# Kernel tuning notes

Hardware: AMD Instinct MI355X
Metric: run time of the kernel (lower is better)

The kernel has to match this reference:

```python
import jax, jax.numpy as jnp
import numpy as np

B, S, D = 16, 1, 2048
NH, NKV = 32, 8
HD = D // NH          # 64
GRP = NH // NKV       # 4
MAX_SEQ = 4096
START = MAX_SEQ - S   # 4095
HIDDEN = 5632         # 256*ceil((2*4*D/3)/256)
EPS = 1e-6


def _rope(x, cos, sin):
    # x: [b, s, h, d]; cos/sin: [s, d//2]; llama complex rotation on pairs
    b, s, h, d = x.shape
    xr = x.reshape(b, s, h, d // 2, 2)
    x0, x1 = xr[..., 0], xr[..., 1]
    c = cos[None, :, None, :]
    sn = sin[None, :, None, :]
    o0 = x0 * c - x1 * sn
    o1 = x0 * sn + x1 * c
    return jnp.stack([o0, o1], axis=-1).reshape(b, s, h, d)


def _rmsnorm(x, w, eps=EPS):
    return w * (x * jax.lax.rsqrt(jnp.mean(x * x, axis=-1, keepdims=True) + eps))


def setup_inputs() -> dict:
    key = jax.random.key(0)
    ks = jax.random.split(key, 12)
    sc = 0.02
    pos = jnp.arange(START, START + S, dtype=jnp.float32)
    inv = 1.0 / (10000.0 ** (jnp.arange(0, HD, 2, dtype=jnp.float32) / HD))
    ang = pos[:, None] * inv[None, :]  # [S, HD//2]
    return {
        "x": jax.random.normal(ks[0], (B, S, D), jnp.float32),
        "freqs_cos": jnp.cos(ang),
        "freqs_sin": jnp.sin(ang),
        "cache_k": jax.random.normal(ks[1], (B, MAX_SEQ, NKV, HD), jnp.float32),
        "cache_v": jax.random.normal(ks[2], (B, MAX_SEQ, NKV, HD), jnp.float32),
        "wq_w": jax.random.normal(ks[3], (D, D), jnp.float32) * sc,
        "wk_w": jax.random.normal(ks[4], (NKV * HD, D), jnp.float32) * sc,
        "wv_w": jax.random.normal(ks[5], (NKV * HD, D), jnp.float32) * sc,
        "wo_w": jax.random.normal(ks[6], (D, D), jnp.float32) * sc,
        "w1_w": jax.random.normal(ks[7], (HIDDEN, D), jnp.float32) * sc,
        "w2_w": jax.random.normal(ks[8], (D, HIDDEN), jnp.float32) * sc,
        "w3_w": jax.random.normal(ks[9], (D, D), jnp.float32) * sc,
        "attn_norm_w": jnp.ones((D,), jnp.float32),
        "ffn_norm_w": jnp.ones((D,), jnp.float32),
        "start_pos": START,
    }


def reference(x, freqs_cos, freqs_sin, cache_k, cache_v, wq_w, wk_w, wv_w, wo_w,
              w1_w, w2_w, w3_w, attn_norm_w, ffn_norm_w, start_pos):
    b, s, dim = x.shape
    # --- attention ---
    xn = _rmsnorm(x, attn_norm_w)
    xq = (xn @ wq_w.T).reshape(b, s, NH, HD)
    xk = (xn @ wk_w.T).reshape(b, s, NKV, HD)
    xv = (xn @ wv_w.T).reshape(b, s, NKV, HD)
    # source applies rotary embedding to q, k AND v
    xq = _rope(xq, freqs_cos, freqs_sin)
    xk = _rope(xk, freqs_cos, freqs_sin)
    xv = _rope(xv, freqs_cos, freqs_sin)
    # KV-cache write at start_pos, read prefix
    cache_k = jax.lax.dynamic_update_slice(cache_k, xk, (0, start_pos, 0, 0))
    cache_v = jax.lax.dynamic_update_slice(cache_v, xv, (0, start_pos, 0, 0))
    T = start_pos + s
    keys = cache_k[:, :T]   # [b, T, NKV, HD]
    vals = cache_v[:, :T]
    # GQA: group q heads per kv head (equivalent to repeat_kv + matmul)
    q = xq.reshape(b, s, NKV, GRP, HD)
    scores = jnp.einsum('bsKgd,btKd->bKgst', q, keys) / jnp.sqrt(jnp.float32(HD))
    probs = jax.nn.softmax(scores.astype(jnp.float32), axis=-1).astype(xq.dtype)
    attn = jnp.einsum('bKgst,btKd->bsKgd', probs, vals).reshape(b, s, dim)
    h = x + attn @ wo_w.T
    hn = _rmsnorm(h, ffn_norm_w)
    ff = jax.nn.silu(hn @ w1_w.T) @ w2_w.T + hn @ w3_w.T
    return h + ff
```

## Files before the change

### kernel.cpp

```cpp
#include <hip/hip_runtime.h>
#include <math.h>

#define NB      16
#define DIM     2048
#define NKVh    8
#define HDIM    64
#define GRP     4
#define MAXSEQ  4096
#define TPOS    4095
#define FFH     5632
#define NSPLIT  8
#define CHUNK   512

#define XN_OFF   0
#define Q_OFF    32768
#define ATTN_OFF 65536
#define H_OFF    98304
#define HN_OFF   131072
#define H1_OFF   163840
#define H3_OFF   253952
#define PML_OFF  286720
#define PO_OFF   294912

__global__ __launch_bounds__(256) void rmsnorm_k(const float* __restrict__ x,
    const float* __restrict__ w, float* __restrict__ o) {
  int b = blockIdx.x;
  const float* xr = x + b * DIM;
  float ss = 0.f;
#pragma unroll
  for (int i = 0; i < DIM / 256; ++i) {
    float v = xr[threadIdx.x + i * 256];
    ss += v * v;
  }
#pragma unroll
  for (int m = 32; m >= 1; m >>= 1) ss += __shfl_xor(ss, m, 64);
  __shared__ float sred[4];
  if ((threadIdx.x & 63) == 0) sred[threadIdx.x >> 6] = ss;
  __syncthreads();
  float r = rsqrtf((sred[0] + sred[1] + sred[2] + sred[3]) * (1.f / DIM) + 1e-6f);
#pragma unroll
  for (int i = 0; i < DIM / 256; ++i) {
    int idx = threadIdx.x + i * 256;
    o[b * DIM + idx] = w[idx] * xr[idx] * r;
  }
}

template <int K4>
__device__ inline void gemv_core(const float* __restrict__ W,
                                 const float* __restrict__ X,
                                 int row0, float acc[4][4]) {
  const int lane = threadIdx.x & 63;
  const int wv   = threadIdx.x >> 6;
  const int lk   = lane & 15;
  const int b4   = lane >> 4;
  const float4* __restrict__ Wv = (const float4*)W;
  const float4* __restrict__ Xv = (const float4*)X;
#pragma unroll
  for (int r = 0; r < 4; ++r)
#pragma unroll
    for (int j = 0; j < 4; ++j) acc[r][j] = 0.f;

  const int half = K4 / 2;
  int k4 = wv * half + lk;
#pragma unroll 2
  for (int i = 0; i < half / 16; ++i, k4 += 16) {
    float4 xb[4];
#pragma unroll
    for (int j = 0; j < 4; ++j) xb[j] = Xv[(b4 + 4 * j) * K4 + k4];
#pragma unroll
    for (int r = 0; r < 4; ++r) {
      float4 wr = Wv[(row0 + r) * K4 + k4];
#pragma unroll
      for (int j = 0; j < 4; ++j)
        acc[r][j] += wr.x * xb[j].x + wr.y * xb[j].y + wr.z * xb[j].z + wr.w * xb[j].w;
    }
  }
#pragma unroll
  for (int m = 1; m < 16; m <<= 1)
#pragma unroll
    for (int r = 0; r < 4; ++r)
#pragma unroll
      for (int j = 0; j < 4; ++j) acc[r][j] += __shfl_xor(acc[r][j], m, 64);
  __shared__ float sred[4][4][4];
  if (wv == 1 && lk == 0) {
#pragma unroll
    for (int r = 0; r < 4; ++r)
#pragma unroll
      for (int j = 0; j < 4; ++j) sred[b4][r][j] = acc[r][j];
  }
  __syncthreads();
  if (wv == 0) {
#pragma unroll
    for (int r = 0; r < 4; ++r)
#pragma unroll
      for (int j = 0; j < 4; ++j) acc[r][j] += sred[b4][r][j];
  }
}

__global__ __launch_bounds__(128) void qkv_k(const float* __restrict__ xn,
    const float* __restrict__ wq, const float* __restrict__ wk,
    const float* __restrict__ wv, const float* __restrict__ fc,
    const float* __restrict__ fs, float* __restrict__ qo,
    float* __restrict__ ck, float* __restrict__ cv) {
  int row0 = blockIdx.x * 4;
  const float* W;
  int lr, kind;
  if (row0 < DIM)            { W = wq; lr = row0;             kind = 0; }
  else if (row0 < DIM + 512) { W = wk; lr = row0 - DIM;       kind = 1; }
  else                       { W = wv; lr = row0 - DIM - 512; kind = 2; }
  float acc[4][4];
  gemv_core<512>(W, xn, lr, acc);
  if ((threadIdx.x >> 6) != 0 || (threadIdx.x & 15) != 0) return;
  int b4 = (threadIdx.x >> 4) & 3;
  int dl = lr & 63;
  int j0 = dl >> 1;
  float c0 = fc[j0], s0 = fs[j0], c1 = fc[j0 + 1], s1 = fs[j0 + 1];
  const float QS = 0.125f * 1.44269504088896f;
#pragma unroll
  for (int j = 0; j < 4; ++j) {
    int b = b4 + 4 * j;
    float a0 = acc[0][j], a1 = acc[1][j], a2 = acc[2][j], a3 = acc[3][j];
    float o0 = a0 * c0 - a1 * s0, o1 = a0 * s0 + a1 * c0;
    float o2 = a2 * c1 - a3 * s1, o3 = a2 * s1 + a3 * c1;
    if (kind == 0) {
      float* qp = qo + b * DIM + lr;
      qp[0] = o0 * QS; qp[1] = o1 * QS; qp[2] = o2 * QS; qp[3] = o3 * QS;
    } else {
      int kvh = lr >> 6;
      float* cp = (kind == 1 ? ck : cv) +
                  (((size_t)b * MAXSEQ + TPOS) * NKVh + kvh) * HDIM + dl;
      cp[0] = o0; cp[1] = o1; cp[2] = o2; cp[3] = o3;
    }
  }
}

__global__ __launch_bounds__(256) void attn_part_k(const float* __restrict__ q,
    const float* __restrict__ ck, const float* __restrict__ cv,
    float* __restrict__ pml, float* __restrict__ po) {
  int blk = blockIdx.x;
  int sp = blk & (NSPLIT - 1);
  int bk = blk / NSPLIT;
  int kv = bk & 7, b = bk >> 3;
  int w = threadIdx.x >> 6, lane = threadIdx.x & 63;
  int tg = lane >> 4, lk = lane & 15;

  float4 q4[GRP];
#pragma unroll
  for (int g = 0; g < GRP; ++g)
    q4[g] = *(const float4*)&q[b * DIM + (kv * GRP + g) * HDIM + lk * 4];

  float m[GRP], l[GRP];
  float4 o[GRP];
#pragma unroll
  for (int g = 0; g < GRP; ++g) {
    m[g] = -1e30f; l[g] = 0.f;
    o[g].x = 0.f; o[g].y = 0.f; o[g].z = 0.f; o[g].w = 0.f;
  }
  const float4* Kb = (const float4*)ck + (size_t)b * (MAXSEQ * NKVh * HDIM / 4) + kv * (HDIM / 4);
  const float4* Vb = (const float4*)cv + (size_t)b * (MAXSEQ * NKVh * HDIM / 4) + kv * (HDIM / 4);
  int t0 = sp * CHUNK + w * 4 + tg;
#pragma unroll 2
  for (int it = 0; it < CHUNK / 16; ++it) {
    int t = t0 + it * 16;
    float4 kr = Kb[(size_t)t * (NKVh * HDIM / 4) + lk];
    float s[GRP];
#pragma unroll
    for (int g = 0; g < GRP; ++g)
      s[g] = kr.x * q4[g].x + kr.y * q4[g].y + kr.z * q4[g].z + kr.w * q4[g].w;
#pragma unroll
    for (int msk = 1; msk < 16; msk <<= 1)
#pragma unroll
      for (int g = 0; g < GRP; ++g) s[g] += __shfl_xor(s[g], msk, 64);
    float4 vr = Vb[(size_t)t * (NKVh * HDIM / 4) + lk];
#pragma unroll
    for (int g = 0; g < GRP; ++g) {
      float mn = fmaxf(m[g], s[g]);
      float sc = exp2f(m[g] - mn);
      float p  = exp2f(s[g] - mn);
      l[g] = l[g] * sc + p;
      o[g].x = o[g].x * sc + p * vr.x;
      o[g].y = o[g].y * sc + p * vr.y;
      o[g].z = o[g].z * sc + p * vr.z;
      o[g].w = o[g].w * sc + p * vr.w;
      m[g] = mn;
    }
  }
  __shared__ float sml[16][GRP][2];
  __shared__ float so[16][GRP][HDIM];
  int set = w * 4 + tg;
#pragma unroll
  for (int g = 0; g < GRP; ++g) {
    *(float4*)&so[set][g][lk * 4] = o[g];
    if (lk == 0) { sml[set][g][0] = m[g]; sml[set][g][1] = l[g]; }
  }
  __syncthreads();
  int g = threadIdx.x >> 6, d = threadIdx.x & 63;
  float M = -1e30f;
#pragma unroll
  for (int s2 = 0; s2 < 16; ++s2) M = fmaxf(M, sml[s2][g][0]);
  float L = 0.f, O = 0.f;
#pragma unroll
  for (int s2 = 0; s2 < 16; ++s2) {
    float e = exp2f(sml[s2][g][0] - M);
    L += e * sml[s2][g][1];
    O += e * so[s2][g][d];
  }
  int idx = (bk * GRP + g) * NSPLIT + sp;
  po[idx * HDIM + d] = O;
  if (d == 0) { pml[idx * 2] = M; pml[idx * 2 + 1] = L; }
}

__global__ __launch_bounds__(256) void attn_comb_k(const float* __restrict__ pml,
    const float* __restrict__ po, float* __restrict__ attn) {
  int t = blockIdx.x * 256 + threadIdx.x;
  int d = t & 63, bkg = t >> 6;
  float M = -1e30f;
#pragma unroll
  for (int sp = 0; sp < NSPLIT; ++sp) M = fmaxf(M, pml[(bkg * NSPLIT + sp) * 2]);
  float L = 0.f, O = 0.f;
#pragma unroll
  for (int sp = 0; sp < NSPLIT; ++sp) {
    float e = exp2f(pml[(bkg * NSPLIT + sp) * 2] - M);
    L += e * pml[(bkg * NSPLIT + sp) * 2 + 1];
    O += e * po[(bkg * NSPLIT + sp) * HDIM + d];
  }
  attn[bkg * HDIM + d] = O / L;
}

__global__ __launch_bounds__(128) void wo_k(const float* __restrict__ attn,
    const float* __restrict__ wo, const float* __restrict__ x,
    float* __restrict__ h) {
  int row0 = blockIdx.x * 4;
  float acc[4][4];
  gemv_core<512>(wo, attn, row0, acc);
  if ((threadIdx.x >> 6) != 0 || (threadIdx.x & 15) != 0) return;
  int b4 = (threadIdx.x >> 4) & 3;
#pragma unroll
  for (int j = 0; j < 4; ++j) {
    int b = b4 + 4 * j;
#pragma unroll
    for (int r = 0; r < 4; ++r)
      h[b * DIM + row0 + r] = x[b * DIM + row0 + r] + acc[r][j];
  }
}

__global__ __launch_bounds__(128) void ffn13_k(const float* __restrict__ hn,
    const float* __restrict__ w1, const float* __restrict__ w3,
    float* __restrict__ h1, float* __restrict__ h3) {
  int row0 = blockIdx.x * 4;
  bool is1 = row0 < FFH;
  const float* W = is1 ? w1 : w3;
  int lr = is1 ? row0 : row0 - FFH;
  float acc[4][4];
  gemv_core<512>(W, hn, lr, acc);
  if ((threadIdx.x >> 6) != 0 || (threadIdx.x & 15) != 0) return;
  int b4 = (threadIdx.x >> 4) & 3;
#pragma unroll
  for (int j = 0; j < 4; ++j) {
    int b = b4 + 4 * j;
#pragma unroll
    for (int r = 0; r < 4; ++r) {
      float v = acc[r][j];
      if (is1) h1[b * FFH + lr + r] = v / (1.f + expf(-v));
      else     h3[b * DIM + lr + r] = v;
    }
  }
}

__global__ __launch_bounds__(128) void ffn2_k(const float* __restrict__ h1,
    const float* __restrict__ w2, const float* __restrict__ h,
    const float* __restrict__ h3, float* __restrict__ out) {
  int row0 = blockIdx.x * 4;
  float acc[4][4];
  gemv_core<1408>(w2, h1, row0, acc);
  if ((threadIdx.x >> 6) != 0 || (threadIdx.x & 15) != 0) return;
  int b4 = (threadIdx.x >> 4) & 3;
#pragma unroll
  for (int j = 0; j < 4; ++j) {
    int b = b4 + 4 * j;
#pragma unroll
    for (int r = 0; r < 4; ++r)
      out[b * DIM + row0 + r] = h[b * DIM + row0 + r] + h3[b * DIM + row0 + r] + acc[r][j];
  }
}

extern "C" void kernel_launch(void* const* d_in, const int* in_sizes, int n_in,
                              void* d_out, int out_size, void* d_ws, size_t ws_size,
                              hipStream_t stream) {
  (void)in_sizes; (void)n_in; (void)out_size; (void)ws_size;
  const float* x   = (const float*)d_in[0];
  const float* fc  = (const float*)d_in[1];
  const float* fs  = (const float*)d_in[2];
  float*       ck  = (float*)d_in[3];
  float*       cv  = (float*)d_in[4];
  const float* wq  = (const float*)d_in[5];
  const float* wk  = (const float*)d_in[6];
  const float* wvp = (const float*)d_in[7];
  const float* wo  = (const float*)d_in[8];
  const float* w1  = (const float*)d_in[9];
  const float* w2  = (const float*)d_in[10];
  const float* w3  = (const float*)d_in[11];
  const float* anw = (const float*)d_in[12];
  const float* fnw = (const float*)d_in[13];
  float* ws  = (float*)d_ws;
  float* out = (float*)d_out;

  rmsnorm_k<<<NB, 256, 0, stream>>>(x, anw, ws + XN_OFF);
  qkv_k<<<(DIM + 512 + 512) / 4, 128, 0, stream>>>(ws + XN_OFF, wq, wk, wvp, fc, fs,
                                                   ws + Q_OFF, ck, cv);
  attn_part_k<<<NB * NKVh * NSPLIT, 256, 0, stream>>>(ws + Q_OFF, ck, cv,
                                                      ws + PML_OFF, ws + PO_OFF);
  attn_comb_k<<<(NB * DIM) / 256, 256, 0, stream>>>(ws + PML_OFF, ws + PO_OFF, ws + ATTN_OFF);
  wo_k<<<DIM / 4, 128, 0, stream>>>(ws + ATTN_OFF, wo, x, ws + H_OFF);
  rmsnorm_k<<<NB, 256, 0, stream>>>(ws + H_OFF, fnw, ws + HN_OFF);
  ffn13_k<<<(FFH + DIM) / 4, 128, 0, stream>>>(ws + HN_OFF, w1, w3, ws + H1_OFF, ws + H3_OFF);
  ffn2_k<<<DIM / 4, 128, 0, stream>>>(ws + H1_OFF, w2, ws + H_OFF, ws + H3_OFF, out);
}
```

Measured before the change: 476.4 us.

## Rework GEMV to single-wave 64-accumulator transpose reduction and widen attention lanes

Replaces the two-wave GEMV core with a single 64-thread wave per 4 rows. Each lane loads contiguous float4 weight chunks and accumulates all 16 batch rows, then uses a butterfly shuffle-transpose reduction so each lane ends with one output, with no shared memory or barrier. QKV, wo and FFN kernels now launch 64-thread blocks, and the RoPE epilogue uses a lane shuffle. Attention partials now assign 8 lanes per token with 8 dims each, giving a shorter shuffle reduction and 32 partial sets, at the cost of higher register pressure from 64 accumulators and fewer waves per block.

```diff
diff --git a/kernel.cpp b/kernel.cpp
--- a/kernel.cpp
+++ b/kernel.cpp
@@ -22,6 +22,10 @@
 #define PML_OFF  286720
 #define PO_OFF   294912
 
+__device__ __forceinline__ float dot4(float4 a, float4 b) {
+  return a.x * b.x + a.y * b.y + a.z * b.z + a.w * b.w;
+}
+
 __global__ __launch_bounds__(256) void rmsnorm_k(const float* __restrict__ x,
     const float* __restrict__ w, float* __restrict__ o) {
   int b = blockIdx.x;
@@ -46,58 +50,46 @@
 }
 
 template <int K4>
-__device__ inline void gemv_core(const float* __restrict__ W,
-                                 const float* __restrict__ X,
-                                 int row0, float acc[4][4]) {
+__device__ __forceinline__ float gemv64(const float* __restrict__ W,
+                                        const float* __restrict__ X, int row0) {
   const int lane = threadIdx.x & 63;
-  const int wv   = threadIdx.x >> 6;
-  const int lk   = lane & 15;
-  const int b4   = lane >> 4;
   const float4* __restrict__ Wv = (const float4*)W;
   const float4* __restrict__ Xv = (const float4*)X;
-#pragma unroll
-  for (int r = 0; r < 4; ++r)
-#pragma unroll
-    for (int j = 0; j < 4; ++j) acc[r][j] = 0.f;
-
-  const int half = K4 / 2;
-  int k4 = wv * half + lk;
+  float a[64];
+#pragma unroll
+  for (int j = 0; j < 64; ++j) a[j] = 0.f;
 #pragma unroll 2
-  for (int i = 0; i < half / 16; ++i, k4 += 16) {
-    float4 xb[4];
-#pragma unroll
-    for (int j = 0; j < 4; ++j) xb[j] = Xv[(b4 + 4 * j) * K4 + k4];
-#pragma unroll
-    for (int r = 0; r < 4; ++r) {
-      float4 wr = Wv[(row0 + r) * K4 + k4];
-#pragma unroll
-      for (int j = 0; j < 4; ++j)
-        acc[r][j] += wr.x * xb[j].x + wr.y * xb[j].y + wr.z * xb[j].z + wr.w * xb[j].w;
+  for (int it = 0; it < K4 / 64; ++it) {
+    int k = it * 64 + lane;
+    float4 w0 = Wv[(size_t)(row0 + 0) * K4 + k];
+    float4 w1 = Wv[(size_t)(row0 + 1) * K4 + k];
+    float4 w2 = Wv[(size_t)(row0 + 2) * K4 + k];
+    float4 w3 = Wv[(size_t)(row0 + 3) * K4 + k];
+#pragma unroll
+    for (int b = 0; b < 16; ++b) {
+      float4 xb = Xv[(size_t)b * K4 + k];
+      a[0 * 16 + b] += dot4(w0, xb);
+      a[1 * 16 + b] += dot4(w1, xb);
+      a[2 * 16 + b] += dot4(w2, xb);
+      a[3 * 16 + b] += dot4(w3, xb);
     }
   }
 #pragma unroll
-  for (int m = 1; m < 16; m <<= 1)
-#pragma unroll
-    for (int r = 0; r < 4; ++r)
-#pragma unroll
-      for (int j = 0; j < 4; ++j) acc[r][j] += __shfl_xor(acc[r][j], m, 64);
-  __shared__ float sred[4][4][4];
-  if (wv == 1 && lk == 0) {
-#pragma unroll
-    for (int r = 0; r < 4; ++r)
-#pragma unroll
-      for (int j = 0; j < 4; ++j) sred[b4][r][j] = acc[r][j];
-  }
-  __syncthreads();
-  if (wv == 0) {
-#pragma unroll
-    for (int r = 0; r < 4; ++r)
-#pragma unroll
-      for (int j = 0; j < 4; ++j) acc[r][j] += sred[b4][r][j];
-  }
-}
-
-__global__ __launch_bounds__(128) void qkv_k(const float* __restrict__ xn,
+  for (int s = 0; s < 6; ++s) {
+    const int m = 1 << s;
+    const int mybit = (lane >> s) & 1;
+#pragma unroll
+    for (int i = 0; i < (64 >> (s + 1)); ++i) {
+      float x0 = a[2 * i], x1 = a[2 * i + 1];
+      float keep = mybit ? x1 : x0;
+      float give = mybit ? x0 : x1;
+      a[i] = keep + __shfl_xor(give, m, 64);
+    }
+  }
+  return a[0];
+}
+
+__global__ __launch_bounds__(64) void qkv_k(const float* __restrict__ xn,
     const float* __restrict__ wq, const float* __restrict__ wk,
     const float* __restrict__ wv, const float* __restrict__ fc,
     const float* __restrict__ fs, float* __restrict__ qo,
@@ -108,29 +100,22 @@
   if (row0 < DIM)            { W = wq; lr = row0;             kind = 0; }
   else if (row0 < DIM + 512) { W = wk; lr = row0 - DIM;       kind = 1; }
   else                       { W = wv; lr = row0 - DIM - 512; kind = 2; }
-  float acc[4][4];
-  gemv_core<512>(W, xn, lr, acc);
-  if ((threadIdx.x >> 6) != 0 || (threadIdx.x & 15) != 0) return;
-  int b4 = (threadIdx.x >> 4) & 3;
-  int dl = lr & 63;
-  int j0 = dl >> 1;
-  float c0 = fc[j0], s0 = fs[j0], c1 = fc[j0 + 1], s1 = fs[j0 + 1];
+  float v = gemv64<512>(W, xn, lr);
+  float pv = __shfl_xor(v, 16, 64);
+  int lane = threadIdx.x & 63;
+  int r = lane >> 4, b = lane & 15;
+  int dl = (lr & 63) + r;
+  int jp = ((lr & 63) + (r & 2)) >> 1;
+  float c = fc[jp], sn = fs[jp];
+  float o = (r & 1) ? (pv * sn + v * c) : (v * c - pv * sn);
   const float QS = 0.125f * 1.44269504088896f;
-#pragma unroll
-  for (int j = 0; j < 4; ++j) {
-    int b = b4 + 4 * j;
-    float a0 = acc[0][j], a1 = acc[1][j], a2 = acc[2][j], a3 = acc[3][j];
-    float o0 = a0 * c0 - a1 * s0, o1 = a0 * s0 + a1 * c0;
-    float o2 = a2 * c1 - a3 * s1, o3 = a2 * s1 + a3 * c1;
-    if (kind == 0) {
-      float* qp = qo + b * DIM + lr;
-      qp[0] = o0 * QS; qp[1] = o1 * QS; qp[2] = o2 * QS; qp[3] = o3 * QS;
-    } else {
-      int kvh = lr >> 6;
-      float* cp = (kind == 1 ? ck : cv) +
-                  (((size_t)b * MAXSEQ + TPOS) * NKVh + kvh) * HDIM + dl;
-      cp[0] = o0; cp[1] = o1; cp[2] = o2; cp[3] = o3;
-    }
+  if (kind == 0) {
+    qo[b * DIM + lr + r] = o * QS;
+  } else {
+    int kvh = lr >> 6;
+    float* cp = (kind == 1 ? ck : cv) +
+                (((size_t)b * MAXSEQ + TPOS) * NKVh + kvh) * HDIM + dl;
+    *cp = o;
   }
 }
 
@@ -142,65 +127,77 @@
   int bk = blk / NSPLIT;
   int kv = bk & 7, b = bk >> 3;
   int w = threadIdx.x >> 6, lane = threadIdx.x & 63;
-  int tg = lane >> 4, lk = lane & 15;
-
-  float4 q4[GRP];
-#pragma unroll
-  for (int g = 0; g < GRP; ++g)
-    q4[g] = *(const float4*)&q[b * DIM + (kv * GRP + g) * HDIM + lk * 4];
+  int t8 = lane >> 3, d8 = lane & 7;
+
+  float4 q4[GRP][2];
+#pragma unroll
+  for (int g = 0; g < GRP; ++g) {
+    const float* qp = q + b * DIM + (kv * GRP + g) * HDIM + d8 * 8;
+    q4[g][0] = *(const float4*)qp;
+    q4[g][1] = *(const float4*)(qp + 4);
+  }
 
   float m[GRP], l[GRP];
-  float4 o[GRP];
+  float4 o0[GRP], o1[GRP];
 #pragma unroll
   for (int g = 0; g < GRP; ++g) {
     m[g] = -1e30f; l[g] = 0.f;
-    o[g].x = 0.f; o[g].y = 0.f; o[g].z = 0.f; o[g].w = 0.f;
-  }
-  const float4* Kb = (const float4*)ck + (size_t)b * (MAXSEQ * NKVh * HDIM / 4) + kv * (HDIM / 4);
-  const float4* Vb = (const float4*)cv + (size_t)b * (MAXSEQ * NKVh * HDIM / 4) + kv * (HDIM / 4);
-  int t0 = sp * CHUNK + w * 4 + tg;
+    o0[g] = make_float4(0.f, 0.f, 0.f, 0.f);
+    o1[g] = make_float4(0.f, 0.f, 0.f, 0.f);
+  }
+  const size_t bkoff = ((size_t)b * MAXSEQ * NKVh + kv) * HDIM + d8 * 8;
+  const float* Kp = ck + bkoff;
+  const float* Vp = cv + bkoff;
+  int tbase = sp * CHUNK + w * 128 + t8;
 #pragma unroll 2
-  for (int it = 0; it < CHUNK / 16; ++it) {
-    int t = t0 + it * 16;
-    float4 kr = Kb[(size_t)t * (NKVh * HDIM / 4) + lk];
+  for (int it = 0; it < 16; ++it) {
+    size_t toff = (size_t)(tbase + it * 8) * (NKVh * HDIM);
+    float4 ka = *(const float4*)(Kp + toff);
+    float4 kb = *(const float4*)(Kp + toff + 4);
     float s[GRP];
 #pragma unroll
     for (int g = 0; g < GRP; ++g)
-      s[g] = kr.x * q4[g].x + kr.y * q4[g].y + kr.z * q4[g].z + kr.w * q4[g].w;
-#pragma unroll
-    for (int msk = 1; msk < 16; msk <<= 1)
+      s[g] = dot4(ka, q4[g][0]) + dot4(kb, q4[g][1]);
+#pragma unroll
+    for (int msk = 1; msk < 8; msk <<= 1)
 #pragma unroll
       for (int g = 0; g < GRP; ++g) s[g] += __shfl_xor(s[g], msk, 64);
-    float4 vr = Vb[(size_t)t * (NKVh * HDIM / 4) + lk];
+    float4 va = *(const float4*)(Vp + toff);
+    float4 vb = *(const float4*)(Vp + toff + 4);
 #pragma unroll
     for (int g = 0; g < GRP; ++g) {
       float mn = fmaxf(m[g], s[g]);
       float sc = exp2f(m[g] - mn);
       float p  = exp2f(s[g] - mn);
       l[g] = l[g] * sc + p;
-      o[g].x = o[g].x * sc + p * vr.x;
-      o[g].y = o[g].y * sc + p * vr.y;
-      o[g].z = o[g].z * sc + p * vr.z;
-      o[g].w = o[g].w * sc + p * vr.w;
+      o0[g].x = o0[g].x * sc + p * va.x;
+      o0[g].y = o0[g].y * sc + p * va.y;
+      o0[g].z = o0[g].z * sc + p * va.z;
+      o0[g].w = o0[g].w * sc + p * va.w;
+      o1[g].x = o1[g].x * sc + p * vb.x;
+      o1[g].y = o1[g].y * sc + p * vb.y;
+      o1[g].z = o1[g].z * sc + p * vb.z;
+      o1[g].w = o1[g].w * sc + p * vb.w;
       m[g] = mn;
     }
   }
-  __shared__ float sml[16][GRP][2];
-  __shared__ float so[16][GRP][HDIM];
-  int set = w * 4 + tg;
+  __shared__ float sml[32][GRP][2];
+  __shared__ float so[32][GRP][HDIM];
+  int set = w * 8 + t8;
 #pragma unroll
   for (int g = 0; g < GRP; ++g) {
-    *(float4*)&so[set][g][lk * 4] = o[g];
-    if (lk == 0) { sml[set][g][0] = m[g]; sml[set][g][1] = l[g]; }
+    *(float4*)&so[set][g][d8 * 8]     = o0[g];
+    *(float4*)&so[set][g][d8 * 8 + 4] = o1[g];
+    if (d8 == 0) { sml[set][g][0] = m[g]; sml[set][g][1] = l[g]; }
   }
   __syncthreads();
   int g = threadIdx.x >> 6, d = threadIdx.x & 63;
   float M = -1e30f;
 #pragma unroll
-  for (int s2 = 0; s2 < 16; ++s2) M = fmaxf(M, sml[s2][g][0]);
+  for (int s2 = 0; s2 < 32; ++s2) M = fmaxf(M, sml[s2][g][0]);
   float L = 0.f, O = 0.f;
 #pragma unroll
-  for (int s2 = 0; s2 < 16; ++s2) {
+  for (int s2 = 0; s2 < 32; ++s2) {
     float e = exp2f(sml[s2][g][0] - M);
     L += e * sml[s2][g][1];
     O += e * so[s2][g][d];
@@ -227,61 +224,38 @@
   attn[bkg * HDIM + d] = O / L;
 }
 
-__global__ __launch_bounds__(128) void wo_k(const float* __restrict__ attn,
+__global__ __launch_bounds__(64) void wo_k(const float* __restrict__ attn,
     const float* __restrict__ wo, const float* __restrict__ x,
     float* __restrict__ h) {
   int row0 = blockIdx.x * 4;
-  float acc[4][4];
-  gemv_core<512>(wo, attn, row0, acc);
-  if ((threadIdx.x >> 6) != 0 || (threadIdx.x & 15) != 0) return;
-  int b4 = (threadIdx.x >> 4) & 3;
-#pragma unroll
-  for (int j = 0; j < 4; ++j) {
-    int b = b4 + 4 * j;
-#pragma unroll
-    for (int r = 0; r < 4; ++r)
-      h[b * DIM + row0 + r] = x[b * DIM + row0 + r] + acc[r][j];
-  }
-}
-
-__global__ __launch_bounds__(128) void ffn13_k(const float* __restrict__ hn,
+  float v = gemv64<512>(wo, attn, row0);
+  int lane = threadIdx.x & 63;
+  int r = lane >> 4, b = lane & 15;
+  h[b * DIM + row0 + r] = x[b * DIM + row0 + r] + v;
+}
+
+__global__ __launch_bounds__(64) void ffn13_k(const float* __restrict__ hn,
     const float* __restrict__ w1, const float* __restrict__ w3,
     float* __restrict__ h1, float* __restrict__ h3) {
   int row0 = blockIdx.x * 4;
   bool is1 = row0 < FFH;
   const float* W = is1 ? w1 : w3;
   int lr = is1 ? row0 : row0 - FFH;
-  float acc[4][4];
-  gemv_core<512>(W, hn, lr, acc);
-  if ((threadIdx.x >> 6) != 0 || (threadIdx.x & 15) != 0) return;
-  int b4 = (threadIdx.x >> 4) & 3;
-#pragma unroll
-  for (int j = 0; j < 4; ++j) {
-    int b = b4 + 4 * j;
-#pragma unroll
-    for (int r = 0; r < 4; ++r) {
-      float v = acc[r][j];
-      if (is1) h1[b * FFH + lr + r] = v / (1.f + expf(-v));
-      else     h3[b * DIM + lr + r] = v;
-    }
-  }
-}
-
-__global__ __launch_bounds__(128) void ffn2_k(const float* __restrict__ h1,
+  float v = gemv64<512>(W, hn, lr);
+  int lane = threadIdx.x & 63;
+  int r = lane >> 4, b = lane & 15;
+  if (is1) h1[b * FFH + lr + r] = v / (1.f + expf(-v));
+  else     h3[b * DIM + lr + r] = v;
+}
+
+__global__ __launch_bounds__(64) void ffn2_k(const float* __restrict__ h1,
     const float* __restrict__ w2, const float* __restrict__ h,
     const float* __restrict__ h3, float* __restrict__ out) {
   int row0 = blockIdx.x * 4;
-  float acc[4][4];
-  gemv_core<1408>(w2, h1, row0, acc);
-  if ((threadIdx.x >> 6) != 0 || (threadIdx.x & 15) != 0) return;
-  int b4 = (threadIdx.x >> 4) & 3;
-#pragma unroll
-  for (int j = 0; j < 4; ++j) {
-    int b = b4 + 4 * j;
-#pragma unroll
-    for (int r = 0; r < 4; ++r)
-      out[b * DIM + row0 + r] = h[b * DIM + row0 + r] + h3[b * DIM + row0 + r] + acc[r][j];
-  }
+  float v = gemv64<1408>(w2, h1, row0);
+  int lane = threadIdx.x & 63;
+  int r = lane >> 4, b = lane & 15;
+  out[b * DIM + row0 + r] = h[b * DIM + row0 + r] + h3[b * DIM + row0 + r] + v;
 }
 
 extern "C" void kernel_launch(void* const* d_in, const int* in_sizes, int n_in,
@@ -306,13 +280,13 @@
   float* out = (float*)d_out;
 
   rmsnorm_k<<<NB, 256, 0, stream>>>(x, anw, ws + XN_OFF);
-  qkv_k<<<(DIM + 512 + 512) / 4, 128, 0, stream>>>(ws + XN_OFF, wq, wk, wvp, fc, fs,
-                                                   ws + Q_OFF, ck, cv);
+  qkv_k<<<(DIM + 512 + 512) / 4, 64, 0, stream>>>(ws + XN_OFF, wq, wk, wvp, fc, fs,
+                                                  ws + Q_OFF, ck, cv);
   attn_part_k<<<NB * NKVh * NSPLIT, 256, 0, stream>>>(ws + Q_OFF, ck, cv,
                                                       ws + PML_OFF, ws + PO_OFF);
   attn_comb_k<<<(NB * DIM) / 256, 256, 0, stream>>>(ws + PML_OFF, ws + PO_OFF, ws + ATTN_OFF);
-  wo_k<<<DIM / 4, 128, 0, stream>>>(ws + ATTN_OFF, wo, x, ws + H_OFF);
+  wo_k<<<DIM / 4, 64, 0, stream>>>(ws + ATTN_OFF, wo, x, ws + H_OFF);
   rmsnorm_k<<<NB, 256, 0, stream>>>(ws + H_OFF, fnw, ws + HN_OFF);
-  ffn13_k<<<(FFH + DIM) / 4, 128, 0, stream>>>(ws + HN_OFF, w1, w3, ws + H1_OFF, ws + H3_OFF);
-  ffn2_k<<<DIM / 4, 128, 0, stream>>>(ws + H1_OFF, w2, ws + H_OFF, ws + H3_OFF, out);
-}
+  ffn13_k<<<(FFH + DIM) / 4, 64, 0, stream>>>(ws + HN_OFF, w1, w3, ws + H1_OFF, ws + H3_OFF);
+  ffn2_k<<<DIM / 4, 64, 0, stream>>>(ws + H1_OFF, w2, ws + H_OFF, ws + H3_OFF, out);
+}
```

Measured after the change: 525.2 us. +10.3%, slower.

## Stage KV cache through LDS with async loads and double-buffer GEMV loads

Applied to the files above, without the earlier changes.

Attention partials now run one 512-thread block per (batch, split), covering all 8 KV heads. Each block copies contiguous K/V rows into a 4-deep LDS ring using global_load_lds, overlapping with compute via vmcnt waits and barriers. The GEMV core is rewritten with explicit software pipelining that alternates two register sets of weight and activation loads. The aims are fully coalesced cache reads and hidden memory latency, at the cost of far fewer attention blocks (256), 64KB of LDS per block and more register pressure.

```diff
diff --git a/kernel.cpp b/kernel.cpp
--- a/kernel.cpp
+++ b/kernel.cpp
@@ -9,8 +9,9 @@
 #define MAXSEQ  4096
 #define TPOS    4095
 #define FFH     5632
-#define NSPLIT  8
-#define CHUNK   512
+#define NSPLIT  16
+#define TSPAN   256
+#define TROW    512
 
 #define XN_OFF   0
 #define Q_OFF    32768
@@ -20,7 +21,18 @@
 #define H1_OFF   163840
 #define H3_OFF   253952
 #define PML_OFF  286720
-#define PO_OFF   294912
+#define PO_OFF   303104
+
+__device__ __forceinline__ float dot4(float4 a, float4 b) {
+  return a.x * b.x + a.y * b.y + a.z * b.z + a.w * b.w;
+}
+
+#define GLOAD_LDS(srcp, ldsp)                                                  \
+  __builtin_amdgcn_global_load_lds(                                            \
+      (const __attribute__((address_space(1))) void*)(srcp),                   \
+      (__attribute__((address_space(3))) void*)(ldsp), 16, 0, 0)
+
+#define WAITBAR(N) asm volatile("s_waitcnt vmcnt(" #N ")\n\ts_barrier" ::: "memory")
 
 __global__ __launch_bounds__(256) void rmsnorm_k(const float* __restrict__ x,
     const float* __restrict__ w, float* __restrict__ o) {
@@ -46,9 +58,9 @@
 }
 
 template <int K4>
-__device__ inline void gemv_core(const float* __restrict__ W,
-                                 const float* __restrict__ X,
-                                 int row0, float acc[4][4]) {
+__device__ __forceinline__ void gemv_core(const float* __restrict__ W,
+                                          const float* __restrict__ X,
+                                          int row0, float acc[4][4]) {
   const int lane = threadIdx.x & 63;
   const int wv   = threadIdx.x >> 6;
   const int lk   = lane & 15;
@@ -59,22 +71,41 @@
   for (int r = 0; r < 4; ++r)
 #pragma unroll
     for (int j = 0; j < 4; ++j) acc[r][j] = 0.f;
-
-  const int half = K4 / 2;
-  int k4 = wv * half + lk;
-#pragma unroll 2
-  for (int i = 0; i < half / 16; ++i, k4 += 16) {
-    float4 xb[4];
-#pragma unroll
-    for (int j = 0; j < 4; ++j) xb[j] = Xv[(b4 + 4 * j) * K4 + k4];
-#pragma unroll
-    for (int r = 0; r < 4; ++r) {
-      float4 wr = Wv[(row0 + r) * K4 + k4];
-#pragma unroll
-      for (int j = 0; j < 4; ++j)
-        acc[r][j] += wr.x * xb[j].x + wr.y * xb[j].y + wr.z * xb[j].z + wr.w * xb[j].w;
-    }
-  }
+  constexpr int NI = K4 / 32;
+  const int k0 = wv * (K4 / 2) + lk;
+  float4 aw0, aw1, aw2, aw3, ax0, ax1, ax2, ax3;
+  float4 bw0, bw1, bw2, bw3, bx0, bx1, bx2, bx3;
+#define LDA(S, it) { int kk = k0 + (it) * 16;                                  \
+    S##w0 = Wv[(size_t)(row0 + 0) * K4 + kk];                                  \
+    S##w1 = Wv[(size_t)(row0 + 1) * K4 + kk];                                  \
+    S##w2 = Wv[(size_t)(row0 + 2) * K4 + kk];                                  \
+    S##w3 = Wv[(size_t)(row0 + 3) * K4 + kk];                                  \
+    S##x0 = Xv[(size_t)(b4 + 0) * K4 + kk];                                    \
+    S##x1 = Xv[(size_t)(b4 + 4) * K4 + kk];                                    \
+    S##x2 = Xv[(size_t)(b4 + 8) * K4 + kk];                                    \
+    S##x3 = Xv[(size_t)(b4 + 12) * K4 + kk]; }
+#define FMA4(S) {                                                              \
+    acc[0][0] += dot4(S##w0, S##x0); acc[0][1] += dot4(S##w0, S##x1);          \
+    acc[0][2] += dot4(S##w0, S##x2); acc[0][3] += dot4(S##w0, S##x3);          \
+    acc[1][0] += dot4(S##w1, S##x0); acc[1][1] += dot4(S##w1, S##x1);          \
+    acc[1][2] += dot4(S##w1, S##x2); acc[1][3] += dot4(S##w1, S##x3);          \
+    acc[2][0] += dot4(S##w2, S##x0); acc[2][1] += dot4(S##w2, S##x1);          \
+    acc[2][2] += dot4(S##w2, S##x2); acc[2][3] += dot4(S##w2, S##x3);          \
+    acc[3][0] += dot4(S##w3, S##x0); acc[3][1] += dot4(S##w3, S##x1);          \
+    acc[3][2] += dot4(S##w3, S##x2); acc[3][3] += dot4(S##w3, S##x3); }
+  LDA(a, 0);
+#pragma unroll 1
+  for (int it = 0; it + 2 < NI; it += 2) {
+    LDA(b, it + 1);
+    FMA4(a);
+    LDA(a, it + 2);
+    FMA4(b);
+  }
+  LDA(b, NI - 1);
+  FMA4(a);
+  FMA4(b);
+#undef LDA
+#undef FMA4
 #pragma unroll
   for (int m = 1; m < 16; m <<= 1)
 #pragma unroll
@@ -134,80 +165,106 @@
   }
 }
 
-__global__ __launch_bounds__(256) void attn_part_k(const float* __restrict__ q,
+__global__ __launch_bounds__(512) void attn_part_k(const float* __restrict__ q,
     const float* __restrict__ ck, const float* __restrict__ cv,
     float* __restrict__ pml, float* __restrict__ po) {
-  int blk = blockIdx.x;
-  int sp = blk & (NSPLIT - 1);
-  int bk = blk / NSPLIT;
-  int kv = bk & 7, b = bk >> 3;
-  int w = threadIdx.x >> 6, lane = threadIdx.x & 63;
-  int tg = lane >> 4, lk = lane & 15;
+  __shared__ float smem[16384];
+  int sp = blockIdx.x & (NSPLIT - 1);
+  int b  = blockIdx.x >> 4;
+  int tid = threadIdx.x;
+  int w = tid >> 6, lane = tid & 63;
+  int t4 = lane >> 4, dl = lane & 15;
+
+  const float* Kg = ck + ((size_t)b * MAXSEQ + sp * TSPAN) * TROW;
+  const float* Vg = cv + ((size_t)b * MAXSEQ + sp * TSPAN) * TROW;
+  const float* Sg = (w < 4) ? Kg : Vg;
+  const int    srow = w & 3;
 
   float4 q4[GRP];
 #pragma unroll
   for (int g = 0; g < GRP; ++g)
-    q4[g] = *(const float4*)&q[b * DIM + (kv * GRP + g) * HDIM + lk * 4];
+    q4[g] = *(const float4*)(q + b * DIM + (w * GRP + g) * HDIM + dl * 4);
 
   float m[GRP], l[GRP];
   float4 o[GRP];
 #pragma unroll
   for (int g = 0; g < GRP; ++g) {
     m[g] = -1e30f; l[g] = 0.f;
-    o[g].x = 0.f; o[g].y = 0.f; o[g].z = 0.f; o[g].w = 0.f;
-  }
-  const float4* Kb = (const float4*)ck + (size_t)b * (MAXSEQ * NKVh * HDIM / 4) + kv * (HDIM / 4);
-  const float4* Vb = (const float4*)cv + (size_t)b * (MAXSEQ * NKVh * HDIM / 4) + kv * (HDIM / 4);
-  int t0 = sp * CHUNK + w * 4 + tg;
-#pragma unroll 2
-  for (int it = 0; it < CHUNK / 16; ++it) {
-    int t = t0 + it * 16;
-    float4 kr = Kb[(size_t)t * (NKVh * HDIM / 4) + lk];
-    float s[GRP];
-#pragma unroll
-    for (int g = 0; g < GRP; ++g)
-      s[g] = kr.x * q4[g].x + kr.y * q4[g].y + kr.z * q4[g].z + kr.w * q4[g].w;
-#pragma unroll
-    for (int msk = 1; msk < 16; msk <<= 1)
-#pragma unroll
-      for (int g = 0; g < GRP; ++g) s[g] += __shfl_xor(s[g], msk, 64);
-    float4 vr = Vb[(size_t)t * (NKVh * HDIM / 4) + lk];
-#pragma unroll
-    for (int g = 0; g < GRP; ++g) {
-      float mn = fmaxf(m[g], s[g]);
-      float sc = exp2f(m[g] - mn);
-      float p  = exp2f(s[g] - mn);
-      l[g] = l[g] * sc + p;
-      o[g].x = o[g].x * sc + p * vr.x;
-      o[g].y = o[g].y * sc + p * vr.y;
-      o[g].z = o[g].z * sc + p * vr.z;
-      o[g].w = o[g].w * sc + p * vr.w;
-      m[g] = mn;
+    o[g] = make_float4(0.f, 0.f, 0.f, 0.f);
+  }
+
+#define STAGE(tile) {                                                          \
+    const float* src = Sg + ((size_t)(tile) * 4 + srow) * TROW + lane * 4;     \
+    float* dst = smem + (((tile) & 3) * 4096) + ((w >= 4) ? 2048 : 0) +        \
+                 srow * TROW;                                                  \
+    GLOAD_LDS(src, dst);                                                       \
+    GLOAD_LDS(src + 256, dst + 256); }
+
+#define COMPUTE(tile) {                                                        \
+    const float* bb = smem + (((tile) & 3) * 4096) + t4 * TROW + w * 64 + dl * 4; \
+    float4 ka = *(const float4*)bb;                                            \
+    float4 va = *(const float4*)(bb + 2048);                                   \
+    float s_[GRP];                                                             \
+    _Pragma("unroll") for (int g = 0; g < GRP; ++g) s_[g] = dot4(ka, q4[g]);   \
+    _Pragma("unroll") for (int msk = 1; msk < 16; msk <<= 1)                   \
+      _Pragma("unroll") for (int g = 0; g < GRP; ++g)                          \
+        s_[g] += __shfl_xor(s_[g], msk, 64);                                   \
+    _Pragma("unroll") for (int g = 0; g < GRP; ++g) {                          \
+      float mn = fmaxf(m[g], s_[g]);                                           \
+      float sc = exp2f(m[g] - mn);                                             \
+      float p  = exp2f(s_[g] - mn);                                            \
+      l[g] = l[g] * sc + p;                                                    \
+      o[g].x = o[g].x * sc + p * va.x;                                         \
+      o[g].y = o[g].y * sc + p * va.y;                                         \
+      o[g].z = o[g].z * sc + p * va.z;                                         \
+      o[g].w = o[g].w * sc + p * va.w;                                         \
+      m[g] = mn; } }
+
+  STAGE(0);
+  STAGE(1);
+#pragma unroll 1
+  for (int t = 0; t < 62; ++t) {
+    STAGE(t + 2);
+    WAITBAR(4);
+    COMPUTE(t);
+  }
+  WAITBAR(2);
+  COMPUTE(62);
+  WAITBAR(0);
+  COMPUTE(63);
+#undef STAGE
+#undef COMPUTE
+
+  __syncthreads();
+  float* so  = smem;
+  float* sml = smem + 8192;
+#pragma unroll
+  for (int g = 0; g < GRP; ++g) {
+    *(float4*)&so[(((w * 4 + t4) * GRP) + g) * 64 + dl * 4] = o[g];
+    if (dl == 0) {
+      sml[(((w * 4 + t4) * GRP) + g) * 2]     = m[g];
+      sml[(((w * 4 + t4) * GRP) + g) * 2 + 1] = l[g];
     }
   }
-  __shared__ float sml[16][GRP][2];
-  __shared__ float so[16][GRP][HDIM];
-  int set = w * 4 + tg;
+  __syncthreads();
+  int kv2 = tid >> 6, d = tid & 63;
 #pragma unroll
   for (int g = 0; g < GRP; ++g) {
-    *(float4*)&so[set][g][lk * 4] = o[g];
-    if (lk == 0) { sml[set][g][0] = m[g]; sml[set][g][1] = l[g]; }
-  }
-  __syncthreads();
-  int g = threadIdx.x >> 6, d = threadIdx.x & 63;
-  float M = -1e30f;
-#pragma unroll
-  for (int s2 = 0; s2 < 16; ++s2) M = fmaxf(M, sml[s2][g][0]);
-  float L = 0.f, O = 0.f;
-#pragma unroll
-  for (int s2 = 0; s2 < 16; ++s2) {
-    float e = exp2f(sml[s2][g][0] - M);
-    L += e * sml[s2][g][1];
-    O += e * so[s2][g][d];
-  }
-  int idx = (bk * GRP + g) * NSPLIT + sp;
-  po[idx * HDIM + d] = O;
-  if (d == 0) { pml[idx * 2] = M; pml[idx * 2 + 1] = L; }
+    float M = -1e30f;
+#pragma unroll
+    for (int s2 = 0; s2 < 4; ++s2)
+      M = fmaxf(M, sml[(((kv2 * 4 + s2) * GRP) + g) * 2]);
+    float L = 0.f, O = 0.f;
+#pragma unroll
+    for (int s2 = 0; s2 < 4; ++s2) {
+      float e = exp2f(sml[(((kv2 * 4 + s2) * GRP) + g) * 2] - M);
+      L += e * sml[(((kv2 * 4 + s2) * GRP) + g) * 2 + 1];
+      O += e * so[(((kv2 * 4 + s2) * GRP) + g) * 64 + d];
+    }
+    int idx = ((b * NKVh + kv2) * GRP + g) * NSPLIT + sp;
+    po[idx * HDIM + d] = O;
+    if (d == 0) { pml[idx * 2] = M; pml[idx * 2 + 1] = L; }
+  }
 }
 
 __global__ __launch_bounds__(256) void attn_comb_k(const float* __restrict__ pml,
@@ -308,8 +365,8 @@
   rmsnorm_k<<<NB, 256, 0, stream>>>(x, anw, ws + XN_OFF);
   qkv_k<<<(DIM + 512 + 512) / 4, 128, 0, stream>>>(ws + XN_OFF, wq, wk, wvp, fc, fs,
                                                    ws + Q_OFF, ck, cv);
-  attn_part_k<<<NB * NKVh * NSPLIT, 256, 0, stream>>>(ws + Q_OFF, ck, cv,
-                                                      ws + PML_OFF, ws + PO_OFF);
+  attn_part_k<<<NB * NSPLIT, 512, 0, stream>>>(ws + Q_OFF, ck, cv,
+                                               ws + PML_OFF, ws + PO_OFF);
   attn_comb_k<<<(NB * DIM) / 256, 256, 0, stream>>>(ws + PML_OFF, ws + PO_OFF, ws + ATTN_OFF);
   wo_k<<<DIM / 4, 128, 0, stream>>>(ws + ATTN_OFF, wo, x, ws + H_OFF);
   rmsnorm_k<<<NB, 256, 0, stream>>>(ws + H_OFF, fnw, ws + HN_OFF);
```

Result: no change. 467.7 us (-1.8%).
